# Performance work log

Measured on AMD Instinct MI355X. Metric: run time of the kernel, lower is better.

## Reference

```python
import jax, jax.numpy as jnp
import numpy as np

SEQ_LEN, BATCH, VOCAB, EMB, HID, NLAYERS = 64, 128, 10000, 1024, 1024, 2


def setup_inputs() -> dict:
    key = jax.random.key(0)
    ks = jax.random.split(key, 12)
    u = lambda k, shape: jax.random.uniform(k, shape, jnp.float32, -0.1, 0.1)
    inputs = jax.random.randint(ks[0], (SEQ_LEN, BATCH), 0, VOCAB)
    hidden = jnp.zeros((NLAYERS, BATCH, HID), jnp.float32)
    emb_table = u(ks[1], (VOCAB, EMB))
    # gate weights: in_features = EMB(+)HID == 2*HID since EMB==HID; stacked over layers
    Wr = u(ks[2], (NLAYERS, 2 * HID, HID)); br = jnp.zeros((NLAYERS, HID), jnp.float32)
    Wz = u(ks[3], (NLAYERS, 2 * HID, HID)); bz = jnp.zeros((NLAYERS, HID), jnp.float32)
    Wg = u(ks[4], (NLAYERS, 2 * HID, HID)); bg = jnp.zeros((NLAYERS, HID), jnp.float32)
    Wout = u(ks[5], (HID, VOCAB)); bout = jnp.zeros((VOCAB,), jnp.float32)
    return {"inputs": inputs, "hidden": hidden, "emb_table": emb_table,
            "Wr": Wr, "br": br, "Wz": Wz, "bz": bz, "Wg": Wg, "bg": bg,
            "Wout": Wout, "bout": bout}


def reference(inputs, hidden, emb_table, Wr, br, Wz, bz, Wg, bg, Wout, bout):
    # inputs: [T, B] int ids; hidden: [L, B, H]
    x = emb_table[inputs]  # [T, B, E]
    L = Wr.shape[0]

    def step(h, x_t):
        inp = x_t
        new_h = []
        for l in range(L):
            cat = jnp.concatenate([inp, h[l]], axis=-1)            # [B, 2H]
            r = jnp.tanh(cat @ Wr[l] + br[l])                      # tanh gate (as in source)
            z = jnp.tanh(cat @ Wz[l] + bz[l])
            cat2 = jnp.concatenate([inp, r * h[l]], axis=-1)
            h_tild = jnp.tanh(cat2 @ Wg[l] + bg[l])
            hn = (1.0 - z) * h[l] + z * h_tild
            inp = hn
            new_h.append(hn)
        logits_t = jnp.tanh(inp @ Wout + bout)                     # Tanh on logits (as in source)
        return jnp.stack(new_h), logits_t

    h_final, logits = jax.lax.scan(step, hidden, x)
    return logits, h_final
```

## Files before the change

### kernel.cpp

```cpp
#include <hip/hip_runtime.h>

#define T_STEPS 64
#define BATCH   128
#define HID     1024
#define VOCAB   10000
#define VPAD    10240
#define NSPLIT  8
#define KCHUNK  256

typedef unsigned short ushort_t;
typedef __attribute__((ext_vector_type(8))) short bf16x8_t;
typedef __attribute__((ext_vector_type(4))) float f32x4_t;

__device__ inline unsigned short f2bf(float f) {
    unsigned int u = __float_as_uint(f);
    u += 0x7fffu + ((u >> 16) & 1u);
    return (unsigned short)(u >> 16);
}

__global__ void init_h(const float* __restrict__ hidden,
                       float* __restrict__ h0, float* __restrict__ h1)
{
    int i = blockIdx.x * blockDim.x + threadIdx.x;
    if (i < BATCH * HID) {
        h0[i] = hidden[i];
        h1[i] = hidden[BATCH * HID + i];
    }
}

__global__ void final_h(const float* __restrict__ h0, const float* __restrict__ h1,
                        float* __restrict__ out)
{
    int i = blockIdx.x * blockDim.x + threadIdx.x;
    if (i < BATCH * HID) {
        out[i] = h0[i];
        out[BATCH * HID + i] = h1[i];
    }
}

__global__ __launch_bounds__(256)
void gather_kernel(const int* __restrict__ ids, const float* __restrict__ emb,
                   float* __restrict__ xemb)
{
    const int row = blockIdx.x;
    const int c4 = threadIdx.x * 4;
    float4 v = *(const float4*)&emb[(size_t)ids[row] * HID + c4];
    *(float4*)&xemb[(size_t)row * HID + c4] = v;
}

__global__ __launch_bounds__(256)
void woutT_kernel(const float* __restrict__ Wout, ushort_t* __restrict__ WT)
{
    __shared__ float ld[32][33];
    const int v0 = blockIdx.x * 32, k0 = blockIdx.y * 32;
    const int r = threadIdx.x >> 3;
    const int c4 = (threadIdx.x & 7) * 4;
    #pragma unroll
    for (int q = 0; q < 4; ++q) {
        int v = v0 + c4 + q;
        float val = 0.0f;
        if (v < VOCAB) val = Wout[(size_t)(k0 + r) * VOCAB + v];
        ld[c4 + q][r] = val;
    }
    __syncthreads();
    ushort4 o;
    o.x = f2bf(ld[r][c4 + 0]);
    o.y = f2bf(ld[r][c4 + 1]);
    o.z = f2bf(ld[r][c4 + 2]);
    o.w = f2bf(ld[r][c4 + 3]);
    *(ushort4*)&WT[(size_t)(v0 + r) * HID + k0 + c4] = o;
}

__global__ __launch_bounds__(256)
void agemm_kernel(const float* __restrict__ xemb_t0,
                  const float* __restrict__ h0, const float* __restrict__ h1,
                  const float* __restrict__ Wr, const float* __restrict__ Wz,
                  float* __restrict__ part_rz, int do0, int do1)
{
    const int layer = blockIdx.z;
    if (layer == 0 && !do0) return;
    if (layer == 1 && !do1) return;

    __shared__ float As[128][68];
    __shared__ float Bs[64][68];
    const int tid = threadIdx.x;
    const int tx8 = (tid & 7) * 8;
    const int ty  = tid >> 3;
    const int j0 = blockIdx.x * 64;
    const int kbase = blockIdx.y * KCHUNK;

    const float* W = ((j0 < HID) ? Wr : Wz) + (size_t)layer * (2 * HID * HID);
    const int jc = j0 & (HID - 1);
    const float* A_lo = layer ? h0 : xemb_t0;
    const float* A_hi = layer ? h1 : h0;

    float acc[4][8] = {};

    for (int kt0 = 0; kt0 < KCHUNK; kt0 += 64) {
        const int kt = kbase + kt0;
        #pragma unroll
        for (int i = 0; i < 8; ++i) {
            int f = i * 256 + tid;
            int r = f >> 4;
            int c4 = (f & 15) * 4;
            int kg = kt + c4;
            const float* src = (kg < HID) ? A_lo : A_hi;
            *(float4*)&As[r][c4] =
                *(const float4*)&src[(size_t)r * HID + (kg & (HID - 1))];
        }
        #pragma unroll
        for (int i = 0; i < 4; ++i) {
            int f = i * 256 + tid;
            int r = f >> 4;
            int c4 = (f & 15) * 4;
            *(float4*)&Bs[r][c4] =
                *(const float4*)&W[(size_t)(kt + r) * HID + jc + c4];
        }
        __syncthreads();
        #pragma unroll
        for (int kk4 = 0; kk4 < 64; kk4 += 4) {
            float4 a[4], b0[4], b1[4];
            #pragma unroll
            for (int i = 0; i < 4; ++i)
                a[i] = *(const float4*)&As[ty + i * 32][kk4];
            #pragma unroll
            for (int q = 0; q < 4; ++q) {
                b0[q] = *(const float4*)&Bs[kk4 + q][tx8];
                b1[q] = *(const float4*)&Bs[kk4 + q][tx8 + 4];
            }
            #pragma unroll
            for (int q = 0; q < 4; ++q) {
                #pragma unroll
                for (int i = 0; i < 4; ++i) {
                    acc[i][0] += a[i][q] * b0[q][0];
                    acc[i][1] += a[i][q] * b0[q][1];
                    acc[i][2] += a[i][q] * b0[q][2];
                    acc[i][3] += a[i][q] * b0[q][3];
                    acc[i][4] += a[i][q] * b1[q][0];
                    acc[i][5] += a[i][q] * b1[q][1];
                    acc[i][6] += a[i][q] * b1[q][2];
                    acc[i][7] += a[i][q] * b1[q][3];
                }
            }
        }
        __syncthreads();
    }

    float* dst = part_rz + (size_t)(layer * NSPLIT + blockIdx.y) * (BATCH * 2 * HID);
    #pragma unroll
    for (int i = 0; i < 4; ++i) {
        int b = ty + i * 32;
        float4 v0, v1;
        v0.x = acc[i][0]; v0.y = acc[i][1]; v0.z = acc[i][2]; v0.w = acc[i][3];
        v1.x = acc[i][4]; v1.y = acc[i][5]; v1.z = acc[i][6]; v1.w = acc[i][7];
        *(float4*)&dst[(size_t)b * 2048 + j0 + tx8]     = v0;
        *(float4*)&dst[(size_t)b * 2048 + j0 + tx8 + 4] = v1;
    }
}

__global__ __launch_bounds__(256)
void aact_kernel(const float* __restrict__ part_rz,
                 const float* __restrict__ br,
                 float* __restrict__ rmat0, float* __restrict__ rmat1,
                 int do0, int do1)
{
    const int layer = blockIdx.y;
    if (layer == 0 && !do0) return;
    if (layer == 1 && !do1) return;
    const int idx4 = (blockIdx.x * 256 + threadIdx.x) * 4;
    const int b = idx4 >> 10, j = idx4 & (HID - 1);
    const float* p = part_rz + (size_t)layer * NSPLIT * (BATCH * 2 * HID)
                   + (size_t)b * 2048 + j;
    float4 s = {0.f, 0.f, 0.f, 0.f};
    #pragma unroll
    for (int sp = 0; sp < NSPLIT; ++sp) {
        float4 v = *(const float4*)&p[(size_t)sp * (BATCH * 2 * HID)];
        s.x += v.x; s.y += v.y; s.z += v.z; s.w += v.w;
    }
    float4 bb = *(const float4*)&br[layer * HID + j];
    float4 r;
    r.x = tanhf(s.x + bb.x); r.y = tanhf(s.y + bb.y);
    r.z = tanhf(s.z + bb.z); r.w = tanhf(s.w + bb.w);
    *(float4*)&(layer ? rmat1 : rmat0)[idx4] = r;
}

__global__ __launch_bounds__(256)
void bgemm_kernel(const float* __restrict__ xemb_t0,
                  const float* __restrict__ h0, const float* __restrict__ h1,
                  const float* __restrict__ rmat0, const float* __restrict__ rmat1,
                  const float* __restrict__ Wg,
                  float* __restrict__ part_g, int do0, int do1)
{
    const int layer = blockIdx.z;
    if (layer == 0 && !do0) return;
    if (layer == 1 && !do1) return;

    __shared__ float As[128][68];
    __shared__ float Bs[64][36];
    const int tid = threadIdx.x;
    const int tx4 = (tid & 7) * 4;
    const int ty  = tid >> 3;
    const int j0 = blockIdx.x * 32;
    const int kbase = blockIdx.y * KCHUNK;

    const float* W = Wg + (size_t)layer * (2 * HID * HID);
    const float* A_lo = layer ? h0 : xemb_t0;
    const float* A_hi = layer ? h1 : h0;
    const float* R    = layer ? rmat1 : rmat0;

    float acc[4][4] = {};

    for (int kt0 = 0; kt0 < KCHUNK; kt0 += 64) {
        const int kt = kbase + kt0;
        #pragma unroll
        for (int i = 0; i < 8; ++i) {
            int f = i * 256 + tid;
            int r = f >> 4;
            int c4 = (f & 15) * 4;
            int kg = kt + c4;
            int km = kg & (HID - 1);
            float4 v;
            if (kg < HID) {
                v = *(const float4*)&A_lo[(size_t)r * HID + km];
            } else {
                float4 rv = *(const float4*)&R[(size_t)r * HID + km];
                float4 hv = *(const float4*)&A_hi[(size_t)r * HID + km];
                v.x = rv.x * hv.x; v.y = rv.y * hv.y;
                v.z = rv.z * hv.z; v.w = rv.w * hv.w;
            }
            *(float4*)&As[r][c4] = v;
        }
        #pragma unroll
        for (int i = 0; i < 2; ++i) {
            int f = i * 256 + tid;
            int r = f >> 3;
            int c4 = (f & 7) * 4;
            *(float4*)&Bs[r][c4] =
                *(const float4*)&W[(size_t)(kt + r) * HID + j0 + c4];
        }
        __syncthreads();
        #pragma unroll
        for (int kk4 = 0; kk4 < 64; kk4 += 4) {
            float4 a[4], b[4];
            #pragma unroll
            for (int i = 0; i < 4; ++i)
                a[i] = *(const float4*)&As[ty + i * 32][kk4];
            #pragma unroll
            for (int q = 0; q < 4; ++q)
                b[q] = *(const float4*)&Bs[kk4 + q][tx4];
            #pragma unroll
            for (int q = 0; q < 4; ++q) {
                #pragma unroll
                for (int i = 0; i < 4; ++i) {
                    acc[i][0] += a[i][q] * b[q].x;
                    acc[i][1] += a[i][q] * b[q].y;
                    acc[i][2] += a[i][q] * b[q].z;
                    acc[i][3] += a[i][q] * b[q].w;
                }
            }
        }
        __syncthreads();
    }

    float* dst = part_g + (size_t)(layer * NSPLIT + blockIdx.y) * (BATCH * HID);
    #pragma unroll
    for (int i = 0; i < 4; ++i) {
        int b = ty + i * 32;
        float4 v;
        v.x = acc[i][0]; v.y = acc[i][1]; v.z = acc[i][2]; v.w = acc[i][3];
        *(float4*)&dst[(size_t)b * HID + j0 + tx4] = v;
    }
}

__global__ __launch_bounds__(256)
void bact_kernel(const float* __restrict__ part_rz, const float* __restrict__ part_g,
                 const float* __restrict__ bz, const float* __restrict__ bg,
                 float* __restrict__ h0, float* __restrict__ h1,
                 ushort_t* __restrict__ h1bf, int t1, int do0, int do1)
{
    const int layer = blockIdx.y;
    if (layer == 0 && !do0) return;
    if (layer == 1 && !do1) return;
    const int idx4 = (blockIdx.x * 256 + threadIdx.x) * 4;
    const int b = idx4 >> 10, j = idx4 & (HID - 1);

    const float* pz = part_rz + (size_t)layer * NSPLIT * (BATCH * 2 * HID)
                    + (size_t)b * 2048 + HID + j;
    float4 sz = {0.f, 0.f, 0.f, 0.f};
    #pragma unroll
    for (int sp = 0; sp < NSPLIT; ++sp) {
        float4 v = *(const float4*)&pz[(size_t)sp * (BATCH * 2 * HID)];
        sz.x += v.x; sz.y += v.y; sz.z += v.z; sz.w += v.w;
    }
    float4 bzv = *(const float4*)&bz[layer * HID + j];
    float4 z;
    z.x = tanhf(sz.x + bzv.x); z.y = tanhf(sz.y + bzv.y);
    z.z = tanhf(sz.z + bzv.z); z.w = tanhf(sz.w + bzv.w);

    const float* pg = part_g + (size_t)layer * NSPLIT * (BATCH * HID) + idx4;
    float4 sg = {0.f, 0.f, 0.f, 0.f};
    #pragma unroll
    for (int sp = 0; sp < NSPLIT; ++sp) {
        float4 v = *(const float4*)&pg[(size_t)sp * (BATCH * HID)];
        sg.x += v.x; sg.y += v.y; sg.z += v.z; sg.w += v.w;
    }
    float4 bgv = *(const float4*)&bg[layer * HID + j];
    float4 g;
    g.x = tanhf(sg.x + bgv.x); g.y = tanhf(sg.y + bgv.y);
    g.z = tanhf(sg.z + bgv.z); g.w = tanhf(sg.w + bgv.w);

    float* h = layer ? h1 : h0;
    float4 hv = *(const float4*)&h[idx4];
    float4 hn;
    hn.x = (1.0f - z.x) * hv.x + z.x * g.x;
    hn.y = (1.0f - z.y) * hv.y + z.y * g.y;
    hn.z = (1.0f - z.z) * hv.z + z.z * g.z;
    hn.w = (1.0f - z.w) * hv.w + z.w * g.w;
    *(float4*)&h[idx4] = hn;

    if (layer == 1) {
        ushort4 o;
        o.x = f2bf(hn.x); o.y = f2bf(hn.y); o.z = f2bf(hn.z); o.w = f2bf(hn.w);
        *(ushort4*)&h1bf[(size_t)t1 * (BATCH * HID) + idx4] = o;
    }
}

typedef const unsigned int __attribute__((address_space(1)))* gptr1_t;
typedef unsigned int __attribute__((address_space(3)))* lptr3_t;

__global__ __launch_bounds__(256)
void logits_mfma_kernel(const ushort_t* __restrict__ Abf,
                        const ushort_t* __restrict__ BT,
                        const float* __restrict__ bout,
                        float* __restrict__ out)
{
    __shared__ ushort_t As[128 * 64];
    __shared__ ushort_t Bs[128 * 64];
    const int tid = threadIdx.x;
    const int wave = tid >> 6, lane = tid & 63;
    const int m0 = blockIdx.y * 128, n0 = blockIdx.x * 128;
    const int wr = wave >> 1, wc = wave & 1;

    const int srow = lane >> 3;
    const int sch = (lane & 7) ^ (srow & 7);
    const int lrow = lane & 15, lhi = lane >> 4;

    f32x4_t acc[4][4] = {};

    for (int k0 = 0; k0 < HID; k0 += 64) {
        #pragma unroll
        for (int i = 0; i < 4; ++i) {
            int issue = wave * 4 + i;
            int row = issue * 8 + srow;
            const ushort_t* ga = Abf + (size_t)(m0 + row) * HID + k0 + sch * 8;
            const ushort_t* gb = BT + (size_t)(n0 + row) * HID + k0 + sch * 8;
#if defined(__has_builtin) && __has_builtin(__builtin_amdgcn_global_load_lds)
            __builtin_amdgcn_global_load_lds((gptr1_t)(const void*)ga,
                                             (lptr3_t)(void*)(As + issue * 512), 16, 0, 0);
            __builtin_amdgcn_global_load_lds((gptr1_t)(const void*)gb,
                                             (lptr3_t)(void*)(Bs + issue * 512), 16, 0, 0);
#else
            *(bf16x8_t*)(As + issue * 512 + lane * 8) = *(const bf16x8_t*)ga;
            *(bf16x8_t*)(Bs + issue * 512 + lane * 8) = *(const bf16x8_t*)gb;
#endif
        }
        __syncthreads();

        bf16x8_t af[4][2], bfm[4][2];
        const char* Ab = (const char*)As;
        const char* Bb = (const char*)Bs;
        #pragma unroll
        for (int m = 0; m < 4; ++m) {
            int row = wr * 64 + m * 16 + lrow;
            #pragma unroll
            for (int ks = 0; ks < 2; ++ks) {
                int off = row * 128 + (((ks * 4 + lhi) ^ (lrow & 7)) * 16);
                af[m][ks] = *(const bf16x8_t*)(Ab + off);
            }
        }
        #pragma unroll
        for (int n = 0; n < 4; ++n) {
            int row = wc * 64 + n * 16 + lrow;
            #pragma unroll
            for (int ks = 0; ks < 2; ++ks) {
                int off = row * 128 + (((ks * 4 + lhi) ^ (lrow & 7)) * 16);
                bfm[n][ks] = *(const bf16x8_t*)(Bb + off);
            }
        }
        #pragma unroll
        for (int m = 0; m < 4; ++m)
            #pragma unroll
            for (int n = 0; n < 4; ++n)
                #pragma unroll
                for (int ks = 0; ks < 2; ++ks)
                    acc[m][n] = __builtin_amdgcn_mfma_f32_16x16x32_bf16(
                        af[m][ks], bfm[n][ks], acc[m][n], 0, 0, 0);
        __syncthreads();
    }

    #pragma unroll
    for (int m = 0; m < 4; ++m) {
        int row = m0 + wr * 64 + m * 16 + lhi * 4;
        #pragma unroll
        for (int n = 0; n < 4; ++n) {
            int col = n0 + wc * 64 + n * 16 + lrow;
            if (col < VOCAB) {
                float bo = bout[col];
                #pragma unroll
                for (int q = 0; q < 4; ++q)
                    out[(size_t)(row + q) * VOCAB + col] = tanhf(acc[m][n][q] + bo);
            }
        }
    }
}

extern "C" void kernel_launch(void* const* d_in, const int* in_sizes, int n_in,
                              void* d_out, int out_size, void* d_ws, size_t ws_size,
                              hipStream_t stream)
{
    const int*   inputs = (const int*)  d_in[0];
    const float* hidden = (const float*)d_in[1];
    const float* emb    = (const float*)d_in[2];
    const float* Wr     = (const float*)d_in[3];
    const float* br     = (const float*)d_in[4];
    const float* Wz     = (const float*)d_in[5];
    const float* bz     = (const float*)d_in[6];
    const float* Wg     = (const float*)d_in[7];
    const float* bg     = (const float*)d_in[8];
    const float* Wout   = (const float*)d_in[9];
    const float* bout   = (const float*)d_in[10];
    float* out = (float*)d_out;

    const size_t BH = BATCH * HID;

    float* ws = (float*)d_ws;
    float* h0      = ws;
    float* h1      = h0 + BH;
    float* rmat0   = h1 + BH;
    float* rmat1   = rmat0 + BH;
    float* part_rz = rmat1 + BH;
    float* part_g  = part_rz + 2 * NSPLIT * (BATCH * 2 * HID);
    float* xemb    = part_g + 2 * NSPLIT * (BATCH * HID);
    ushort_t* h1bf = (ushort_t*)(xemb + (size_t)T_STEPS * BH);
    ushort_t* WT   = h1bf + (size_t)T_STEPS * BH;

    init_h<<<(int)(BH + 255) / 256, 256, 0, stream>>>(hidden, h0, h1);
    gather_kernel<<<T_STEPS * BATCH, 256, 0, stream>>>(inputs, emb, xemb);
    woutT_kernel<<<dim3(VPAD / 32, HID / 32), 256, 0, stream>>>(Wout, WT);

    for (int s = 0; s <= T_STEPS; ++s) {
        int do0 = (s < T_STEPS) ? 1 : 0;
        int do1 = (s >= 1) ? 1 : 0;
        const float* xemb_t0 = xemb + (size_t)s * BH;
        agemm_kernel<<<dim3(32, NSPLIT, 2), 256, 0, stream>>>(
            xemb_t0, h0, h1, Wr, Wz, part_rz, do0, do1);
        aact_kernel<<<dim3(128, 2), 256, 0, stream>>>(
            part_rz, br, rmat0, rmat1, do0, do1);
        bgemm_kernel<<<dim3(32, NSPLIT, 2), 256, 0, stream>>>(
            xemb_t0, h0, h1, rmat0, rmat1, Wg, part_g, do0, do1);
        bact_kernel<<<dim3(128, 2), 256, 0, stream>>>(
            part_rz, part_g, bz, bg, h0, h1, h1bf, s - 1, do0, do1);
    }

    final_h<<<(int)(BH + 255) / 256, 256, 0, stream>>>(
        h0, h1, out + (size_t)T_STEPS * BATCH * VOCAB);

    logits_mfma_kernel<<<dim3(VPAD / 128, 8192 / 128), 256, 0, stream>>>(
        h1bf, WT, bout, out);
}
```

Measured before the change: 4.643 ms.

## Fuse per-step recurrence kernels into one persistent cooperative kernel with grid syncs

Replaces the 65×4 separate kernel launches of the GRU recurrence with a single cooperative kernel of 256 blocks × 512 threads. It loops over time steps and separates the r/z GEMM, r activation, candidate GEMM, and state update phases with grid.sync(). This is meant to remove launch overhead and inter-kernel gaps. In exchange, the whole recurrence runs on a fixed 256-block grid with four grid barriers per step, and the GEMM tiling is changed. It falls back to the old multi-kernel loop if the cooperative launch fails.

```diff
diff --git a/kernel.cpp b/kernel.cpp
--- a/kernel.cpp
+++ b/kernel.cpp
@@ -1,4 +1,7 @@
 #include <hip/hip_runtime.h>
+#include <hip/hip_cooperative_groups.h>
+
+namespace cg = cooperative_groups;
 
 #define T_STEPS 64
 #define BATCH   128
@@ -69,6 +72,273 @@
     o.z = f2bf(ld[r][c4 + 2]);
     o.w = f2bf(ld[r][c4 + 3]);
     *(ushort4*)&WT[(size_t)(v0 + r) * HID + k0 + c4] = o;
+}
+
+__global__ __launch_bounds__(512)
+void recurrence_coop(const float* __restrict__ xemb,
+                     float* __restrict__ h0, float* __restrict__ h1,
+                     float* __restrict__ rmat0, float* __restrict__ rmat1,
+                     float* __restrict__ part_rz, float* __restrict__ part_g,
+                     ushort_t* __restrict__ h1bf,
+                     const float* __restrict__ Wr, const float* __restrict__ Wz,
+                     const float* __restrict__ Wg,
+                     const float* __restrict__ br, const float* __restrict__ bz,
+                     const float* __restrict__ bg)
+{
+    cg::grid_group grid = cg::this_grid();
+
+    __shared__ float As[128][36];
+    __shared__ float Bs[32][132];
+
+    const int bid = blockIdx.x;
+    const int tid = threadIdx.x;
+
+    for (int s = 0; s <= T_STEPS; ++s) {
+        const int do0 = (s < T_STEPS) ? 1 : 0;
+        const int do1 = (s >= 1) ? 1 : 0;
+        const float* xemb_s = xemb + (size_t)s * (BATCH * HID);
+
+        {
+            const int layer = bid >> 7;
+            const int ok = layer ? do1 : do0;
+            if (ok) {
+                const int j0 = (bid & 15) * 128;
+                const int split = (bid >> 4) & 7;
+                const int kbase = split * KCHUNK;
+                const int tx8 = (tid & 15) * 8;
+                const int ty  = tid >> 4;
+                const float* W = ((j0 < HID) ? Wr : Wz)
+                               + (size_t)layer * (2 * HID * HID);
+                const int jc = j0 & (HID - 1);
+                const float* A_lo = layer ? h0 : xemb_s;
+                const float* A_hi = layer ? h1 : h0;
+
+                float acc[4][8] = {};
+
+                for (int kt0 = 0; kt0 < KCHUNK; kt0 += 32) {
+                    const int kt = kbase + kt0;
+                    #pragma unroll
+                    for (int i = 0; i < 2; ++i) {
+                        int f = i * 512 + tid;
+                        int r = f >> 3;
+                        int c4 = (f & 7) * 4;
+                        int kg = kt + c4;
+                        const float* src = (kg < HID) ? A_lo : A_hi;
+                        *(float4*)&As[r][c4] =
+                            *(const float4*)&src[(size_t)r * HID + (kg & (HID - 1))];
+                    }
+                    #pragma unroll
+                    for (int i = 0; i < 2; ++i) {
+                        int f = i * 512 + tid;
+                        int r = f >> 5;
+                        int c4 = (f & 31) * 4;
+                        *(float4*)&Bs[r][c4] =
+                            *(const float4*)&W[(size_t)(kt + r) * HID + jc + c4];
+                    }
+                    __syncthreads();
+                    #pragma unroll
+                    for (int kk4 = 0; kk4 < 32; kk4 += 4) {
+                        float4 a[4], b0[4], b1[4];
+                        #pragma unroll
+                        for (int i = 0; i < 4; ++i)
+                            a[i] = *(const float4*)&As[ty + i * 32][kk4];
+                        #pragma unroll
+                        for (int q = 0; q < 4; ++q) {
+                            b0[q] = *(const float4*)&Bs[kk4 + q][tx8];
+                            b1[q] = *(const float4*)&Bs[kk4 + q][tx8 + 4];
+                        }
+                        #pragma unroll
+                        for (int q = 0; q < 4; ++q) {
+                            #pragma unroll
+                            for (int i = 0; i < 4; ++i) {
+                                acc[i][0] += a[i][q] * b0[q][0];
+                                acc[i][1] += a[i][q] * b0[q][1];
+                                acc[i][2] += a[i][q] * b0[q][2];
+                                acc[i][3] += a[i][q] * b0[q][3];
+                                acc[i][4] += a[i][q] * b1[q][0];
+                                acc[i][5] += a[i][q] * b1[q][1];
+                                acc[i][6] += a[i][q] * b1[q][2];
+                                acc[i][7] += a[i][q] * b1[q][3];
+                            }
+                        }
+                    }
+                    __syncthreads();
+                }
+
+                float* dst = part_rz
+                    + (size_t)(layer * NSPLIT + split) * (BATCH * 2 * HID);
+                #pragma unroll
+                for (int i = 0; i < 4; ++i) {
+                    int b = ty + i * 32;
+                    float4 v0, v1;
+                    v0.x = acc[i][0]; v0.y = acc[i][1]; v0.z = acc[i][2]; v0.w = acc[i][3];
+                    v1.x = acc[i][4]; v1.y = acc[i][5]; v1.z = acc[i][6]; v1.w = acc[i][7];
+                    *(float4*)&dst[(size_t)b * 2048 + j0 + tx8]     = v0;
+                    *(float4*)&dst[(size_t)b * 2048 + j0 + tx8 + 4] = v1;
+                }
+            }
+        }
+        grid.sync();
+
+        {
+            const unsigned u = bid * 512 + tid;
+            if (u < 65536u) {
+                const int layer = u >> 15;
+                const int ok = layer ? do1 : do0;
+                if (ok) {
+                    const int idx4 = (int)(u & 32767u) * 4;
+                    const int b = idx4 >> 10, j = idx4 & (HID - 1);
+                    const float* p = part_rz + (size_t)layer * NSPLIT * (BATCH * 2 * HID)
+                                   + (size_t)b * 2048 + j;
+                    float4 sv = {0.f, 0.f, 0.f, 0.f};
+                    #pragma unroll
+                    for (int sp = 0; sp < NSPLIT; ++sp) {
+                        float4 v = *(const float4*)&p[(size_t)sp * (BATCH * 2 * HID)];
+                        sv.x += v.x; sv.y += v.y; sv.z += v.z; sv.w += v.w;
+                    }
+                    float4 bb = *(const float4*)&br[layer * HID + j];
+                    float4 r;
+                    r.x = tanhf(sv.x + bb.x); r.y = tanhf(sv.y + bb.y);
+                    r.z = tanhf(sv.z + bb.z); r.w = tanhf(sv.w + bb.w);
+                    *(float4*)&(layer ? rmat1 : rmat0)[idx4] = r;
+                }
+            }
+        }
+        grid.sync();
+
+        {
+            const int layer = bid >> 7;
+            const int ok = layer ? do1 : do0;
+            if (ok) {
+                const int j0 = (bid & 15) * 64;
+                const int split = (bid >> 4) & 7;
+                const int kbase = split * KCHUNK;
+                const int tx4 = (tid & 15) * 4;
+                const int ty  = tid >> 4;
+                const float* W = Wg + (size_t)layer * (2 * HID * HID);
+                const float* A_lo = layer ? h0 : xemb_s;
+                const float* A_hi = layer ? h1 : h0;
+                const float* R    = layer ? rmat1 : rmat0;
+
+                float acc[4][4] = {};
+
+                for (int kt0 = 0; kt0 < KCHUNK; kt0 += 32) {
+                    const int kt = kbase + kt0;
+                    #pragma unroll
+                    for (int i = 0; i < 2; ++i) {
+                        int f = i * 512 + tid;
+                        int r = f >> 3;
+                        int c4 = (f & 7) * 4;
+                        int kg = kt + c4;
+                        int km = kg & (HID - 1);
+                        float4 v;
+                        if (kg < HID) {
+                            v = *(const float4*)&A_lo[(size_t)r * HID + km];
+                        } else {
+                            float4 rv = *(const float4*)&R[(size_t)r * HID + km];
+                            float4 hv = *(const float4*)&A_hi[(size_t)r * HID + km];
+                            v.x = rv.x * hv.x; v.y = rv.y * hv.y;
+                            v.z = rv.z * hv.z; v.w = rv.w * hv.w;
+                        }
+                        *(float4*)&As[r][c4] = v;
+                    }
+                    {
+                        int r = tid >> 4;
+                        int c4 = (tid & 15) * 4;
+                        *(float4*)&Bs[r][c4] =
+                            *(const float4*)&W[(size_t)(kt + r) * HID + j0 + c4];
+                    }
+                    __syncthreads();
+                    #pragma unroll
+                    for (int kk4 = 0; kk4 < 32; kk4 += 4) {
+                        float4 a[4], b[4];
+                        #pragma unroll
+                        for (int i = 0; i < 4; ++i)
+                            a[i] = *(const float4*)&As[ty + i * 32][kk4];
+                        #pragma unroll
+                        for (int q = 0; q < 4; ++q)
+                            b[q] = *(const float4*)&Bs[kk4 + q][tx4];
+                        #pragma unroll
+                        for (int q = 0; q < 4; ++q) {
+                            #pragma unroll
+                            for (int i = 0; i < 4; ++i) {
+                                acc[i][0] += a[i][q] * b[q].x;
+                                acc[i][1] += a[i][q] * b[q].y;
+                                acc[i][2] += a[i][q] * b[q].z;
+                                acc[i][3] += a[i][q] * b[q].w;
+                            }
+                        }
+                    }
+                    __syncthreads();
+                }
+
+                float* dst = part_g
+                    + (size_t)(layer * NSPLIT + split) * (BATCH * HID);
+                #pragma unroll
+                for (int i = 0; i < 4; ++i) {
+                    int b = ty + i * 32;
+                    float4 v;
+                    v.x = acc[i][0]; v.y = acc[i][1]; v.z = acc[i][2]; v.w = acc[i][3];
+                    *(float4*)&dst[(size_t)b * HID + j0 + tx4] = v;
+                }
+            }
+        }
+        grid.sync();
+
+        {
+            const unsigned u = bid * 512 + tid;
+            if (u < 65536u) {
+                const int layer = u >> 15;
+                const int ok = layer ? do1 : do0;
+                if (ok) {
+                    const int idx4 = (int)(u & 32767u) * 4;
+                    const int b = idx4 >> 10, j = idx4 & (HID - 1);
+
+                    const float* pz = part_rz + (size_t)layer * NSPLIT * (BATCH * 2 * HID)
+                                    + (size_t)b * 2048 + HID + j;
+                    float4 sz = {0.f, 0.f, 0.f, 0.f};
+                    #pragma unroll
+                    for (int sp = 0; sp < NSPLIT; ++sp) {
+                        float4 v = *(const float4*)&pz[(size_t)sp * (BATCH * 2 * HID)];
+                        sz.x += v.x; sz.y += v.y; sz.z += v.z; sz.w += v.w;
+                    }
+                    float4 bzv = *(const float4*)&bz[layer * HID + j];
+                    float4 z;
+                    z.x = tanhf(sz.x + bzv.x); z.y = tanhf(sz.y + bzv.y);
+                    z.z = tanhf(sz.z + bzv.z); z.w = tanhf(sz.w + bzv.w);
+
+                    const float* pg = part_g + (size_t)layer * NSPLIT * (BATCH * HID) + idx4;
+                    float4 sg = {0.f, 0.f, 0.f, 0.f};
+                    #pragma unroll
+                    for (int sp = 0; sp < NSPLIT; ++sp) {
+                        float4 v = *(const float4*)&pg[(size_t)sp * (BATCH * HID)];
+                        sg.x += v.x; sg.y += v.y; sg.z += v.z; sg.w += v.w;
+                    }
+                    float4 bgv = *(const float4*)&bg[layer * HID + j];
+                    float4 g;
+                    g.x = tanhf(sg.x + bgv.x); g.y = tanhf(sg.y + bgv.y);
+                    g.z = tanhf(sg.z + bgv.z); g.w = tanhf(sg.w + bgv.w);
+
+                    float* h = layer ? h1 : h0;
+                    float4 hv = *(const float4*)&h[idx4];
+                    float4 hn;
+                    hn.x = (1.0f - z.x) * hv.x + z.x * g.x;
+                    hn.y = (1.0f - z.y) * hv.y + z.y * g.y;
+                    hn.z = (1.0f - z.z) * hv.z + z.z * g.z;
+                    hn.w = (1.0f - z.w) * hv.w + z.w * g.w;
+                    *(float4*)&h[idx4] = hn;
+
+                    if (layer == 1) {
+                        ushort4 o;
+                        o.x = f2bf(hn.x); o.y = f2bf(hn.y);
+                        o.z = f2bf(hn.z); o.w = f2bf(hn.w);
+                        *(ushort4*)&h1bf[(size_t)(s - 1) * (BATCH * HID) + idx4] = o;
+                    }
+                }
+            }
+        }
+        grid.sync();
+    }
 }
 
 __global__ __launch_bounds__(256)
@@ -448,18 +718,31 @@
     gather_kernel<<<T_STEPS * BATCH, 256, 0, stream>>>(inputs, emb, xemb);
     woutT_kernel<<<dim3(VPAD / 32, HID / 32), 256, 0, stream>>>(Wout, WT);
 
-    for (int s = 0; s <= T_STEPS; ++s) {
-        int do0 = (s < T_STEPS) ? 1 : 0;
-        int do1 = (s >= 1) ? 1 : 0;
-        const float* xemb_t0 = xemb + (size_t)s * BH;
-        agemm_kernel<<<dim3(32, NSPLIT, 2), 256, 0, stream>>>(
-            xemb_t0, h0, h1, Wr, Wz, part_rz, do0, do1);
-        aact_kernel<<<dim3(128, 2), 256, 0, stream>>>(
-            part_rz, br, rmat0, rmat1, do0, do1);
-        bgemm_kernel<<<dim3(32, NSPLIT, 2), 256, 0, stream>>>(
-            xemb_t0, h0, h1, rmat0, rmat1, Wg, part_g, do0, do1);
-        bact_kernel<<<dim3(128, 2), 256, 0, stream>>>(
-            part_rz, part_g, bz, bg, h0, h1, h1bf, s - 1, do0, do1);
+    const float* xemb_c = xemb;
+    void* args[] = {
+        (void*)&xemb_c, (void*)&h0, (void*)&h1,
+        (void*)&rmat0, (void*)&rmat1,
+        (void*)&part_rz, (void*)&part_g, (void*)&h1bf,
+        (void*)&Wr, (void*)&Wz, (void*)&Wg,
+        (void*)&br, (void*)&bz, (void*)&bg
+    };
+    hipError_t cerr = hipLaunchCooperativeKernel(
+        (const void*)recurrence_coop, dim3(256), dim3(512), args, 0, stream);
+
+    if (cerr != hipSuccess) {
+        for (int s = 0; s <= T_STEPS; ++s) {
+            int do0 = (s < T_STEPS) ? 1 : 0;
+            int do1 = (s >= 1) ? 1 : 0;
+            const float* xemb_t0 = xemb + (size_t)s * BH;
+            agemm_kernel<<<dim3(32, NSPLIT, 2), 256, 0, stream>>>(
+                xemb_t0, h0, h1, Wr, Wz, part_rz, do0, do1);
+            aact_kernel<<<dim3(128, 2), 256, 0, stream>>>(
+                part_rz, br, rmat0, rmat1, do0, do1);
+            bgemm_kernel<<<dim3(32, NSPLIT, 2), 256, 0, stream>>>(
+                xemb_t0, h0, h1, rmat0, rmat1, Wg, part_g, do0, do1);
+            bact_kernel<<<dim3(128, 2), 256, 0, stream>>>(
+                part_rz, part_g, bz, bg, h0, h1, h1bf, s - 1, do0, do1);
+        }
     }
 
     final_h<<<(int)(BH + 255) / 256, 256, 0, stream>>>(
```

After: 12.59 ms. +171.2%, slower.

## Fuse split-K reductions into GEMM kernels via last-block atomic counters

Applied to the files above, without the earlier changes.

Removes the separate activation kernels by having the last split-K block of each column tile (found with an atomic counter) reduce the partials and apply tanh, gate and state update. Hidden state is double-buffered across steps so the fused update can write new h while other blocks still read the old one, and z is stored for reuse. This halves the kernel launches per timestep and drops one full-grid pass. In exchange it adds fences and atomics, a memset of the counters, and leaves the final reduction on a few blocks.

```diff
diff --git a/kernel.cpp b/kernel.cpp
--- a/kernel.cpp
+++ b/kernel.cpp
@@ -19,12 +19,12 @@
 }
 
 __global__ void init_h(const float* __restrict__ hidden,
-                       float* __restrict__ h0, float* __restrict__ h1)
+                       float* __restrict__ h0buf0, float* __restrict__ h1buf1)
 {
     int i = blockIdx.x * blockDim.x + threadIdx.x;
     if (i < BATCH * HID) {
-        h0[i] = hidden[i];
-        h1[i] = hidden[BATCH * HID + i];
+        h0buf0[i] = hidden[i];
+        h1buf1[i] = hidden[BATCH * HID + i];
     }
 }
 
@@ -72,10 +72,14 @@
 }
 
 __global__ __launch_bounds__(256)
-void agemm_kernel(const float* __restrict__ xemb_t0,
-                  const float* __restrict__ h0, const float* __restrict__ h1,
-                  const float* __restrict__ Wr, const float* __restrict__ Wz,
-                  float* __restrict__ part_rz, int do0, int do1)
+void agemm_fused(const float* __restrict__ xemb_t0,
+                 const float* __restrict__ h0r, const float* __restrict__ h1r,
+                 const float* __restrict__ Wr, const float* __restrict__ Wz,
+                 const float* __restrict__ br, const float* __restrict__ bz,
+                 float* __restrict__ part_rz,
+                 float* __restrict__ rmat0, float* __restrict__ rmat1,
+                 float* __restrict__ zmat0, float* __restrict__ zmat1,
+                 unsigned int* __restrict__ cnt, int s, int do0, int do1)
 {
     const int layer = blockIdx.z;
     if (layer == 0 && !do0) return;
@@ -91,8 +95,8 @@
 
     const float* W = ((j0 < HID) ? Wr : Wz) + (size_t)layer * (2 * HID * HID);
     const int jc = j0 & (HID - 1);
-    const float* A_lo = layer ? h0 : xemb_t0;
-    const float* A_hi = layer ? h1 : h0;
+    const float* A_lo = layer ? h0r : xemb_t0;
+    const float* A_hi = layer ? h1r : h0r;
 
     float acc[4][8] = {};
 
@@ -156,40 +160,60 @@
         *(float4*)&dst[(size_t)b * 2048 + j0 + tx8]     = v0;
         *(float4*)&dst[(size_t)b * 2048 + j0 + tx8 + 4] = v1;
     }
+
+    __threadfence();
+    __syncthreads();
+    __shared__ int lastflag;
+    if (tid == 0) {
+        unsigned idx = (unsigned)((s * 2 + layer) * 32 + blockIdx.x);
+        unsigned old = atomicAdd(&cnt[idx], 1u);
+        lastflag = (old == NSPLIT - 1);
+    }
+    __syncthreads();
+    if (!lastflag) return;
+    __threadfence();
+
+    const float* pbase = part_rz + (size_t)layer * NSPLIT * (BATCH * 2 * HID);
+    float* rm = layer ? rmat1 : rmat0;
+    float* zm = layer ? zmat1 : zmat0;
+    #pragma unroll
+    for (int i = 0; i < 8; ++i) {
+        int f = i * 256 + tid;
+        int b = f >> 4;
+        int c4 = (f & 15) * 4;
+        int j = j0 + c4;
+        const float* p = pbase + (size_t)b * 2048 + j;
+        float4 sv = {0.f, 0.f, 0.f, 0.f};
+        #pragma unroll
+        for (int sp = 0; sp < NSPLIT; ++sp) {
+            float4 v = *(const float4*)&p[(size_t)sp * (BATCH * 2 * HID)];
+            sv.x += v.x; sv.y += v.y; sv.z += v.z; sv.w += v.w;
+        }
+        if (j < HID) {
+            float4 bb = *(const float4*)&br[layer * HID + j];
+            float4 r;
+            r.x = tanhf(sv.x + bb.x); r.y = tanhf(sv.y + bb.y);
+            r.z = tanhf(sv.z + bb.z); r.w = tanhf(sv.w + bb.w);
+            *(float4*)&rm[(size_t)b * HID + j] = r;
+        } else {
+            float4 bb = *(const float4*)&bz[layer * HID + (j - HID)];
+            float4 z;
+            z.x = tanhf(sv.x + bb.x); z.y = tanhf(sv.y + bb.y);
+            z.z = tanhf(sv.z + bb.z); z.w = tanhf(sv.w + bb.w);
+            *(float4*)&zm[(size_t)b * HID + (j - HID)] = z;
+        }
+    }
 }
 
 __global__ __launch_bounds__(256)
-void aact_kernel(const float* __restrict__ part_rz,
-                 const float* __restrict__ br,
-                 float* __restrict__ rmat0, float* __restrict__ rmat1,
-                 int do0, int do1)
-{
-    const int layer = blockIdx.y;
-    if (layer == 0 && !do0) return;
-    if (layer == 1 && !do1) return;
-    const int idx4 = (blockIdx.x * 256 + threadIdx.x) * 4;
-    const int b = idx4 >> 10, j = idx4 & (HID - 1);
-    const float* p = part_rz + (size_t)layer * NSPLIT * (BATCH * 2 * HID)
-                   + (size_t)b * 2048 + j;
-    float4 s = {0.f, 0.f, 0.f, 0.f};
-    #pragma unroll
-    for (int sp = 0; sp < NSPLIT; ++sp) {
-        float4 v = *(const float4*)&p[(size_t)sp * (BATCH * 2 * HID)];
-        s.x += v.x; s.y += v.y; s.z += v.z; s.w += v.w;
-    }
-    float4 bb = *(const float4*)&br[layer * HID + j];
-    float4 r;
-    r.x = tanhf(s.x + bb.x); r.y = tanhf(s.y + bb.y);
-    r.z = tanhf(s.z + bb.z); r.w = tanhf(s.w + bb.w);
-    *(float4*)&(layer ? rmat1 : rmat0)[idx4] = r;
-}
-
-__global__ __launch_bounds__(256)
-void bgemm_kernel(const float* __restrict__ xemb_t0,
-                  const float* __restrict__ h0, const float* __restrict__ h1,
-                  const float* __restrict__ rmat0, const float* __restrict__ rmat1,
-                  const float* __restrict__ Wg,
-                  float* __restrict__ part_g, int do0, int do1)
+void bgemm_fused(const float* __restrict__ xemb_t0,
+                 const float* __restrict__ h0r, const float* __restrict__ h1r,
+                 float* __restrict__ h0w, float* __restrict__ h1w,
+                 const float* __restrict__ rmat0, const float* __restrict__ rmat1,
+                 const float* __restrict__ zmat0, const float* __restrict__ zmat1,
+                 const float* __restrict__ Wg, const float* __restrict__ bg,
+                 float* __restrict__ part_g, ushort_t* __restrict__ h1bf,
+                 unsigned int* __restrict__ cnt, int s, int do0, int do1)
 {
     const int layer = blockIdx.z;
     if (layer == 0 && !do0) return;
@@ -204,8 +228,8 @@
     const int kbase = blockIdx.y * KCHUNK;
 
     const float* W = Wg + (size_t)layer * (2 * HID * HID);
-    const float* A_lo = layer ? h0 : xemb_t0;
-    const float* A_hi = layer ? h1 : h0;
+    const float* A_lo = layer ? h0r : xemb_t0;
+    const float* A_hi = layer ? h1r : h0r;
     const float* R    = layer ? rmat1 : rmat0;
 
     float acc[4][4] = {};
@@ -270,58 +294,56 @@
         v.x = acc[i][0]; v.y = acc[i][1]; v.z = acc[i][2]; v.w = acc[i][3];
         *(float4*)&dst[(size_t)b * HID + j0 + tx4] = v;
     }
-}
-
-__global__ __launch_bounds__(256)
-void bact_kernel(const float* __restrict__ part_rz, const float* __restrict__ part_g,
-                 const float* __restrict__ bz, const float* __restrict__ bg,
-                 float* __restrict__ h0, float* __restrict__ h1,
-                 ushort_t* __restrict__ h1bf, int t1, int do0, int do1)
-{
-    const int layer = blockIdx.y;
-    if (layer == 0 && !do0) return;
-    if (layer == 1 && !do1) return;
-    const int idx4 = (blockIdx.x * 256 + threadIdx.x) * 4;
-    const int b = idx4 >> 10, j = idx4 & (HID - 1);
-
-    const float* pz = part_rz + (size_t)layer * NSPLIT * (BATCH * 2 * HID)
-                    + (size_t)b * 2048 + HID + j;
-    float4 sz = {0.f, 0.f, 0.f, 0.f};
+
+    __threadfence();
+    __syncthreads();
+    __shared__ int lastflag;
+    if (tid == 0) {
+        unsigned idx = (unsigned)((s * 2 + layer) * 32 + blockIdx.x);
+        unsigned old = atomicAdd(&cnt[idx], 1u);
+        lastflag = (old == NSPLIT - 1);
+    }
+    __syncthreads();
+    if (!lastflag) return;
+    __threadfence();
+
+    const float* pbase = part_g + (size_t)layer * NSPLIT * (BATCH * HID);
+    const float* zm = layer ? zmat1 : zmat0;
+    const float* hr = layer ? h1r : h0r;
+    float* hw = layer ? h1w : h0w;
+    const int t1 = s - 1;
     #pragma unroll
-    for (int sp = 0; sp < NSPLIT; ++sp) {
-        float4 v = *(const float4*)&pz[(size_t)sp * (BATCH * 2 * HID)];
-        sz.x += v.x; sz.y += v.y; sz.z += v.z; sz.w += v.w;
-    }
-    float4 bzv = *(const float4*)&bz[layer * HID + j];
-    float4 z;
-    z.x = tanhf(sz.x + bzv.x); z.y = tanhf(sz.y + bzv.y);
-    z.z = tanhf(sz.z + bzv.z); z.w = tanhf(sz.w + bzv.w);
-
-    const float* pg = part_g + (size_t)layer * NSPLIT * (BATCH * HID) + idx4;
-    float4 sg = {0.f, 0.f, 0.f, 0.f};
-    #pragma unroll
-    for (int sp = 0; sp < NSPLIT; ++sp) {
-        float4 v = *(const float4*)&pg[(size_t)sp * (BATCH * HID)];
-        sg.x += v.x; sg.y += v.y; sg.z += v.z; sg.w += v.w;
-    }
-    float4 bgv = *(const float4*)&bg[layer * HID + j];
-    float4 g;
-    g.x = tanhf(sg.x + bgv.x); g.y = tanhf(sg.y + bgv.y);
-    g.z = tanhf(sg.z + bgv.z); g.w = tanhf(sg.w + bgv.w);
-
-    float* h = layer ? h1 : h0;
-    float4 hv = *(const float4*)&h[idx4];
-    float4 hn;
-    hn.x = (1.0f - z.x) * hv.x + z.x * g.x;
-    hn.y = (1.0f - z.y) * hv.y + z.y * g.y;
-    hn.z = (1.0f - z.z) * hv.z + z.z * g.z;
-    hn.w = (1.0f - z.w) * hv.w + z.w * g.w;
-    *(float4*)&h[idx4] = hn;
-
-    if (layer == 1) {
-        ushort4 o;
-        o.x = f2bf(hn.x); o.y = f2bf(hn.y); o.z = f2bf(hn.z); o.w = f2bf(hn.w);
-        *(ushort4*)&h1bf[(size_t)t1 * (BATCH * HID) + idx4] = o;
+    for (int i = 0; i < 4; ++i) {
+        int f = i * 256 + tid;
+        int b = f >> 3;
+        int c4 = (f & 7) * 4;
+        int j = j0 + c4;
+        const float* p = pbase + (size_t)b * HID + j;
+        float4 sg = {0.f, 0.f, 0.f, 0.f};
+        #pragma unroll
+        for (int sp = 0; sp < NSPLIT; ++sp) {
+            float4 v = *(const float4*)&p[(size_t)sp * (BATCH * HID)];
+            sg.x += v.x; sg.y += v.y; sg.z += v.z; sg.w += v.w;
+        }
+        float4 bgv = *(const float4*)&bg[layer * HID + j];
+        float4 g;
+        g.x = tanhf(sg.x + bgv.x); g.y = tanhf(sg.y + bgv.y);
+        g.z = tanhf(sg.z + bgv.z); g.w = tanhf(sg.w + bgv.w);
+
+        float4 z = *(const float4*)&zm[(size_t)b * HID + j];
+        float4 hv = *(const float4*)&hr[(size_t)b * HID + j];
+        float4 hn;
+        hn.x = (1.0f - z.x) * hv.x + z.x * g.x;
+        hn.y = (1.0f - z.y) * hv.y + z.y * g.y;
+        hn.z = (1.0f - z.z) * hv.z + z.z * g.z;
+        hn.w = (1.0f - z.w) * hv.w + z.w * g.w;
+        *(float4*)&hw[(size_t)b * HID + j] = hn;
+
+        if (layer == 1) {
+            ushort4 o;
+            o.x = f2bf(hn.x); o.y = f2bf(hn.y); o.z = f2bf(hn.z); o.w = f2bf(hn.w);
+            *(ushort4*)&h1bf[(size_t)t1 * (BATCH * HID) + (size_t)b * HID + j] = o;
+        }
     }
 }
 
@@ -434,17 +456,24 @@
     const size_t BH = BATCH * HID;
 
     float* ws = (float*)d_ws;
-    float* h0      = ws;
-    float* h1      = h0 + BH;
-    float* rmat0   = h1 + BH;
+    float* h0buf[2] = { ws,          ws + BH };
+    float* h1buf[2] = { ws + 2 * BH, ws + 3 * BH };
+    float* rmat0   = ws + 4 * BH;
     float* rmat1   = rmat0 + BH;
-    float* part_rz = rmat1 + BH;
+    float* zmat0   = rmat1 + BH;
+    float* zmat1   = zmat0 + BH;
+    float* part_rz = zmat1 + BH;
     float* part_g  = part_rz + 2 * NSPLIT * (BATCH * 2 * HID);
     float* xemb    = part_g + 2 * NSPLIT * (BATCH * HID);
     ushort_t* h1bf = (ushort_t*)(xemb + (size_t)T_STEPS * BH);
     ushort_t* WT   = h1bf + (size_t)T_STEPS * BH;
-
-    init_h<<<(int)(BH + 255) / 256, 256, 0, stream>>>(hidden, h0, h1);
+    unsigned int* cnt1 = (unsigned int*)(WT + (size_t)VPAD * HID);
+    unsigned int* cnt2 = cnt1 + (T_STEPS + 1) * 2 * 32;
+
+    hipMemsetAsync(cnt1, 0, 2 * (T_STEPS + 1) * 2 * 32 * sizeof(unsigned int),
+                   stream);
+
+    init_h<<<(int)(BH + 255) / 256, 256, 0, stream>>>(hidden, h0buf[0], h1buf[1]);
     gather_kernel<<<T_STEPS * BATCH, 256, 0, stream>>>(inputs, emb, xemb);
     woutT_kernel<<<dim3(VPAD / 32, HID / 32), 256, 0, stream>>>(Wout, WT);
 
@@ -452,18 +481,22 @@
         int do0 = (s < T_STEPS) ? 1 : 0;
         int do1 = (s >= 1) ? 1 : 0;
         const float* xemb_t0 = xemb + (size_t)s * BH;
-        agemm_kernel<<<dim3(32, NSPLIT, 2), 256, 0, stream>>>(
-            xemb_t0, h0, h1, Wr, Wz, part_rz, do0, do1);
-        aact_kernel<<<dim3(128, 2), 256, 0, stream>>>(
-            part_rz, br, rmat0, rmat1, do0, do1);
-        bgemm_kernel<<<dim3(32, NSPLIT, 2), 256, 0, stream>>>(
-            xemb_t0, h0, h1, rmat0, rmat1, Wg, part_g, do0, do1);
-        bact_kernel<<<dim3(128, 2), 256, 0, stream>>>(
-            part_rz, part_g, bz, bg, h0, h1, h1bf, s - 1, do0, do1);
+        float* h0r = h0buf[s & 1];
+        float* h0w = h0buf[(s + 1) & 1];
+        float* h1r = h1buf[s & 1];
+        float* h1w = h1buf[(s + 1) & 1];
+
+        agemm_fused<<<dim3(32, NSPLIT, 2), 256, 0, stream>>>(
+            xemb_t0, h0r, h1r, Wr, Wz, br, bz,
+            part_rz, rmat0, rmat1, zmat0, zmat1, cnt1, s, do0, do1);
+
+        bgemm_fused<<<dim3(32, NSPLIT, 2), 256, 0, stream>>>(
+            xemb_t0, h0r, h1r, h0w, h1w, rmat0, rmat1, zmat0, zmat1,
+            Wg, bg, part_g, h1bf, cnt2, s, do0, do1);
     }
 
     final_h<<<(int)(BH + 255) / 256, 256, 0, stream>>>(
-        h0, h1, out + (size_t)T_STEPS * BATCH * VOCAB);
+        h0buf[0], h1buf[1], out + (size_t)T_STEPS * BATCH * VOCAB);
 
     logits_mfma_kernel<<<dim3(VPAD / 128, 8192 / 128), 256, 0, stream>>>(
         h1bf, WT, bout, out);
```

Result: slower. 12.93 ms (+178.5%).
